# Optimization experiments

Hardware: AMD Instinct MI355X
Metric: run time of the kernel (lower is better)

Reference implementation:

```python
import jax, jax.numpy as jnp
import numpy as np

TOP_K = 2


def setup_inputs() -> dict:
    key = jax.random.key(0)
    k1, k2, k3, k4 = jax.random.split(key, 4)
    B, S, D, F, E = 4, 512, 512, 2048, 16
    hidden_states = jax.random.normal(k1, (B, S, D), dtype=jnp.float32)
    gate_weight = jax.random.normal(k2, (E, D), dtype=jnp.float32) * 0.02
    w1 = jax.random.normal(k3, (E, F, D), dtype=jnp.float32) * 0.02
    w2 = jax.random.normal(k4, (E, D, F), dtype=jnp.float32) * 0.02
    return {"hidden_states": hidden_states, "gate_weight": gate_weight, "w1": w1, "w2": w2}


def reference(hidden_states, gate_weight, w1, w2):
    B, S, D = hidden_states.shape
    E = gate_weight.shape[0]
    x = hidden_states.reshape(-1, D)  # [T, D]

    # fused_top_k_routing: logits = x @ Wg^T, top-k, softmax over the k values
    gate_logits = x @ gate_weight.T  # [T, E]
    top_vals, top_idx = jax.lax.top_k(gate_logits, TOP_K)  # [T, k]
    routing_w = jax.nn.softmax(top_vals, axis=-1)  # [T, k]

    # _prepare_expert_inputs: token t goes to expert e iff e in its top-k
    mask = jnp.any(top_idx[:, :, None] == jnp.arange(E)[None, None, :], axis=1)  # [T, E] bool

    # Expert FFN on routed tokens, computed densely over (token, expert) pairs then masked.
    # h[t,e,f] = silu(x_t @ W1_e^T)
    h = jax.nn.silu(jnp.einsum('td,efd->tef', x, w1))  # [T, E, F]
    counts = jnp.sum(mask, axis=0)  # [E]
    h_sum = jnp.einsum('tef,te->ef', h, mask.astype(h.dtype))  # [E, F]
    h_mean = h_sum / jnp.maximum(counts, 1)[:, None].astype(h.dtype)

    # fused_expert_scatter_gather uses expert_outputs[e].mean(dim=0);
    # mean(W2 @ act) = W2 @ mean(act) since W2 is linear.
    y_mean = jnp.einsum('ef,edf->ed', h_mean, w2)  # [E, D]
    y_mean = jnp.where((counts > 0)[:, None], y_mean, 0.0)

    # per-token combine: sum_k w_k * mean_output[expert_k]
    out = jnp.einsum('tk,tkd->td', routing_w, y_mean[top_idx])  # [T, D]
    return out.reshape(B, S, D)
```

## Files before the change

kernel.cpp:

```cpp
#include <hip/hip_runtime.h>

#define NTOK   2048
#define DIM    512
#define FDIM   2048
#define NEXP   16
#define CAP    768
#define BT2    128
#define NTB    (CAP / BT2)

typedef __bf16 bf16x8 __attribute__((ext_vector_type(8)));
typedef __bf16 bf16x4 __attribute__((ext_vector_type(4)));
typedef float  floatx4 __attribute__((ext_vector_type(4)));

#define WS_COUNTS    0
#define WS_ZEROPAGE  1024
#define WS_TOPIDX    4096
#define WS_ROUTW     20480
#define WS_HMEAN     36864
#define WS_YMEAN     167936
#define WS_XG        200704
#define WS_ZERO_BYTES 167936

__device__ __forceinline__ void async_lds16(const void* g, void* l) {
    __builtin_amdgcn_global_load_lds(
        (__attribute__((address_space(1))) void*)(void*)g,
        (__attribute__((address_space(3))) void*)l, 16, 0, 0);
}

__global__ __launch_bounds__(256) void k1_route_gather(
    const float* __restrict__ x, const float* __restrict__ gw,
    int* __restrict__ counts, int* __restrict__ top_idx,
    float* __restrict__ routw, __bf16* __restrict__ Xg)
{
    __shared__ float xt[16 * DIM];
    __shared__ float lg[16][17];
    __shared__ int   gdst[16][2];
    const int tid = threadIdx.x;
    const int t0  = blockIdx.x * 16;

    {
        const float4* src = (const float4*)(x + (size_t)t0 * DIM);
        float4* dst = (float4*)xt;
        #pragma unroll
        for (int i = 0; i < 8; ++i) dst[i * 256 + tid] = src[i * 256 + tid];
    }
    __syncthreads();

    {
        const int tl = tid >> 4, e = tid & 15;
        const float4* xr = (const float4*)(xt + tl * DIM);
        const float4* gr = (const float4*)(gw + e * DIM);
        float acc = 0.f;
        #pragma unroll 8
        for (int j = 0; j < DIM / 4; ++j) {
            float4 a = xr[j], b = gr[j];
            acc += a.x * b.x + a.y * b.y + a.z * b.z + a.w * b.w;
        }
        lg[tl][e] = acc;
    }
    __syncthreads();

    if (tid < 16) {
        const int tl = tid;
        float v0 = -1e30f, v1 = -1e30f; int i0 = 0, i1 = 0;
        #pragma unroll
        for (int e = 0; e < NEXP; ++e) {
            float v = lg[tl][e];
            if (v > v0)      { v1 = v0; i1 = i0; v0 = v; i0 = e; }
            else if (v > v1) { v1 = v;  i1 = e; }
        }
        float e1 = __expf(v1 - v0);
        float w0 = 1.f / (1.f + e1);
        float w1 = 1.f - w0;
        const int t = t0 + tl;
        top_idx[t * 2]     = i0; top_idx[t * 2 + 1] = i1;
        routw[t * 2]       = w0; routw[t * 2 + 1]   = w1;
        int p0 = atomicAdd(counts + i0, 1);
        int p1 = atomicAdd(counts + i1, 1);
        gdst[tl][0] = (p0 < CAP) ? (i0 * CAP + p0) : -1;
        gdst[tl][1] = (p1 < CAP) ? (i1 * CAP + p1) : -1;
    }
    __syncthreads();

    #pragma unroll
    for (int it = 0; it < 16; ++it) {
        int s   = it * 256 + tid;
        int job = s >> 7, el = s & 127;
        int tl  = job >> 1, k = job & 1;
        int dst = gdst[tl][k];
        if (dst >= 0) {
            float4 v = ((const float4*)(xt + tl * DIM))[el];
            bf16x4 o = { (__bf16)v.x, (__bf16)v.y, (__bf16)v.z, (__bf16)v.w };
            *(bf16x4*)(Xg + (size_t)dst * DIM + el * 4) = o;
        }
    }
}

__global__ __launch_bounds__(256) void k2_expert_ffn(
    const float* __restrict__ w1, const __bf16* __restrict__ Xg,
    const int* __restrict__ counts, const __bf16* __restrict__ zp,
    float* __restrict__ hmean)
{
    __shared__ __align__(16) __bf16 w1s[2][8 * 65 * 8];
    __shared__ __align__(16) __bf16 xs[2][8 * 128 * 8];
    __shared__ float hred[64][2];

    const int tid = threadIdx.x;
    const int bid = blockIdx.x;
    const int tb  = bid >> 9;
    const int rem = bid & 511;
    const int e   = rem & 15;
    const int f0  = (rem >> 4) * 64;
    const int cnt = min(counts[e], CAP);
    if (tb * BT2 >= cnt) return;
    const float inv = 1.f / (float)cnt;

    const int wv   = tid >> 6;
    const int lane = tid & 63;
    const int q    = lane >> 4;
    const int l15  = lane & 15;
    const int fsub = (wv & 1) * 32;
    const int tsub = (wv >> 1) * 64;

    const int wfA = tid >> 3,        wgA = tid & 7;
    const int wfB = (256 + tid) >> 3, wgB = (256 + tid) & 7;
    const float* w1rowA = w1 + ((size_t)(e * FDIM + f0 + wfA)) * DIM + wgA * 8;
    const float* w1rowB = w1 + ((size_t)(e * FDIM + f0 + wfB)) * DIM + wgB * 8;

    float4 wa0, wb0, wa1, wb1;

    auto ISSUE_W1 = [&](int c) {
        const float* pA = w1rowA + c * 64;
        const float* pB = w1rowB + c * 64;
        wa0 = ((const float4*)pA)[0]; wb0 = ((const float4*)pA)[1];
        wa1 = ((const float4*)pB)[0]; wb1 = ((const float4*)pB)[1];
    };
    auto WRITE_W1 = [&](int b) {
        bf16x8 v;
        v[0] = (__bf16)wa0.x; v[1] = (__bf16)wa0.y; v[2] = (__bf16)wa0.z; v[3] = (__bf16)wa0.w;
        v[4] = (__bf16)wb0.x; v[5] = (__bf16)wb0.y; v[6] = (__bf16)wb0.z; v[7] = (__bf16)wb0.w;
        *(bf16x8*)(&w1s[b][0] + ((size_t)wgA * 65 + wfA) * 8) = v;
        v[0] = (__bf16)wa1.x; v[1] = (__bf16)wa1.y; v[2] = (__bf16)wa1.z; v[3] = (__bf16)wa1.w;
        v[4] = (__bf16)wb1.x; v[5] = (__bf16)wb1.y; v[6] = (__bf16)wb1.z; v[7] = (__bf16)wb1.w;
        *(bf16x8*)(&w1s[b][0] + ((size_t)wgB * 65 + wfB) * 8) = v;
    };
    auto STAGE_X = [&](int b, int c) {
        __bf16* dst0 = &xs[b][0];
        #pragma unroll
        for (int it = 0; it < 4; ++it) {
            int base = it * 256 + wv * 64;
            int slot = base + lane;
            int kg = slot >> 7, t = slot & 127;
            int r  = tb * BT2 + t;
            const __bf16* src = (r < cnt)
                ? (Xg + ((size_t)(e * CAP + r)) * DIM + c * 64 + kg * 8)
                : zp;
            async_lds16(src, dst0 + (size_t)base * 8);
        }
    };

    ISSUE_W1(0);
    STAGE_X(0, 0);
    WRITE_W1(0);
    __syncthreads();

    floatx4 acc[2][4];
    #pragma unroll
    for (int a = 0; a < 2; ++a)
        #pragma unroll
        for (int b = 0; b < 4; ++b) acc[a][b] = (floatx4)0.f;

    int cur = 0;
    for (int c = 0; c < 8; ++c) {
        if (c < 7) {
            ISSUE_W1(c + 1);
            STAGE_X(cur ^ 1, c + 1);
        }
        const __bf16* wp = &w1s[cur][0];
        const __bf16* xp = &xs[cur][0];
        #pragma unroll
        for (int ks = 0; ks < 2; ++ks) {
            const int kg = ks * 4 + q;
            bf16x8 a0 = *(const bf16x8*)(wp + ((size_t)kg * 65 + fsub + l15) * 8);
            bf16x8 a1 = *(const bf16x8*)(wp + ((size_t)kg * 65 + fsub + 16 + l15) * 8);
            #pragma unroll
            for (int tt = 0; tt < 4; ++tt) {
                bf16x8 bfr = *(const bf16x8*)(xp + ((size_t)kg * 128 + tsub + tt * 16 + l15) * 8);
                acc[0][tt] = __builtin_amdgcn_mfma_f32_16x16x32_bf16(a0, bfr, acc[0][tt], 0, 0, 0);
                acc[1][tt] = __builtin_amdgcn_mfma_f32_16x16x32_bf16(a1, bfr, acc[1][tt], 0, 0, 0);
            }
        }
        if (c < 7) {
            WRITE_W1(cur ^ 1);
            __syncthreads();
            cur ^= 1;
        }
    }

    float hs[8];
    #pragma unroll
    for (int i = 0; i < 8; ++i) hs[i] = 0.f;
    #pragma unroll
    for (int fa = 0; fa < 2; ++fa)
        #pragma unroll
        for (int tt = 0; tt < 4; ++tt)
            #pragma unroll
            for (int r = 0; r < 4; ++r) {
                float v = acc[fa][tt][r];
                hs[fa * 4 + r] += v / (1.f + __expf(-v));
            }

    #pragma unroll
    for (int i = 0; i < 8; ++i) {
        float v = hs[i];
        v += __shfl_xor(v, 1);
        v += __shfl_xor(v, 2);
        v += __shfl_xor(v, 4);
        v += __shfl_xor(v, 8);
        hs[i] = v;
    }
    if (l15 == 0) {
        #pragma unroll
        for (int fa = 0; fa < 2; ++fa)
            #pragma unroll
            for (int r = 0; r < 4; ++r) {
                int row = fsub + fa * 16 + q * 4 + r;
                hred[row][wv >> 1] = hs[fa * 4 + r];
            }
    }
    __syncthreads();
    if (tid < 64)
        atomicAdd(hmean + (size_t)e * FDIM + f0 + tid,
                  (hred[tid][0] + hred[tid][1]) * inv);
}

__global__ __launch_bounds__(256) void k3_ymean(
    const float* __restrict__ w2, const float* __restrict__ hmean,
    const int* __restrict__ counts, float* __restrict__ ymean)
{
    __shared__ float hl[FDIM];
    const int tid = threadIdx.x;
    const int bid = blockIdx.x;
    const int e   = bid >> 7;
    const int d0  = (bid & 127) * 4;

    {
        const float4* hg = (const float4*)(hmean + (size_t)e * FDIM);
        float4* hl4 = (float4*)hl;
        hl4[tid]       = hg[tid];
        hl4[256 + tid] = hg[256 + tid];
    }
    __syncthreads();

    const int wv = tid >> 6, lane = tid & 63;
    const int d = d0 + wv;
    const float4* wr  = (const float4*)(w2 + ((size_t)e * DIM + d) * FDIM);
    const float4* hl4 = (const float4*)hl;
    float acc = 0.f;
    #pragma unroll
    for (int i = 0; i < 8; ++i) {
        float4 a = wr[i * 64 + lane];
        float4 h = hl4[i * 64 + lane];
        acc += a.x * h.x + a.y * h.y + a.z * h.z + a.w * h.w;
    }
    #pragma unroll
    for (int m = 1; m < 64; m <<= 1) acc += __shfl_xor(acc, m);
    if (lane == 0)
        ymean[e * DIM + d] = (counts[e] > 0) ? acc : 0.f;
}

__global__ __launch_bounds__(256) void k4_combine(
    const int* __restrict__ top_idx, const float* __restrict__ routw,
    const float* __restrict__ ymean, float* __restrict__ out)
{
    const int idx = blockIdx.x * 256 + threadIdx.x;
    const int t = idx >> 7;
    const int c = idx & 127;
    const int i0 = top_idx[t * 2], i1 = top_idx[t * 2 + 1];
    const float w0 = routw[t * 2], w1 = routw[t * 2 + 1];
    float4 a = ((const float4*)(ymean + (size_t)i0 * DIM))[c];
    float4 b = ((const float4*)(ymean + (size_t)i1 * DIM))[c];
    float4 o;
    o.x = w0 * a.x + w1 * b.x;
    o.y = w0 * a.y + w1 * b.y;
    o.z = w0 * a.z + w1 * b.z;
    o.w = w0 * a.w + w1 * b.w;
    ((float4*)out)[idx] = o;
}

extern "C" void kernel_launch(void* const* d_in, const int* in_sizes, int n_in,
                              void* d_out, int out_size, void* d_ws, size_t ws_size,
                              hipStream_t stream)
{
    (void)in_sizes; (void)n_in; (void)out_size; (void)ws_size;
    const float* x  = (const float*)d_in[0];
    const float* gw = (const float*)d_in[1];
    const float* w1 = (const float*)d_in[2];
    const float* w2 = (const float*)d_in[3];
    float* out = (float*)d_out;

    char* ws = (char*)d_ws;
    int*    counts  = (int*)   (ws + WS_COUNTS);
    const __bf16* zp = (const __bf16*)(ws + WS_ZEROPAGE);
    int*    top_idx = (int*)   (ws + WS_TOPIDX);
    float*  routw   = (float*) (ws + WS_ROUTW);
    float*  hmean   = (float*) (ws + WS_HMEAN);
    float*  ymean   = (float*) (ws + WS_YMEAN);
    __bf16* Xg      = (__bf16*)(ws + WS_XG);

    hipMemsetAsync(d_ws, 0, WS_ZERO_BYTES, stream);

    k1_route_gather<<<dim3(NTOK / 16), dim3(256), 0, stream>>>(x, gw, counts, top_idx, routw, Xg);
    k2_expert_ffn  <<<dim3(NTB * 32 * NEXP), dim3(256), 0, stream>>>(w1, Xg, counts, zp, hmean);
    k3_ymean       <<<dim3(NEXP * 128), dim3(256), 0, stream>>>(w2, hmean, counts, ymean);
    k4_combine     <<<dim3(NTOK * DIM / 4 / 256), dim3(256), 0, stream>>>(top_idx, routw, ymean, out);
}
```

Measured before the change: 218.4 us.

## Load W1 fragments directly into registers and remap blocks across XCDs

The W1 tile no longer goes through shared memory. Each lane loads its MFMA A-fragment straight from global fp32, converts it to bf16 in registers and feeds the MFMA directly. This removes the LDS store/load round trip and halves LDS usage. In exchange, W1 rows are duplicated across the two t-sub waves that share an f-sub, and global loads become less coalesced (per-lane strided rows). Block indices are also remapped so that the token-blocks of the same (expert, f) tile land on the same XCD, improving L2 reuse of W1.

New measurement: 258.0 us. +18.2%, slower.

```diff
diff --git a/kernel.cpp b/kernel.cpp
--- a/kernel.cpp
+++ b/kernel.cpp
@@ -101,17 +101,19 @@
     const int* __restrict__ counts, const __bf16* __restrict__ zp,
     float* __restrict__ hmean)
 {
-    __shared__ __align__(16) __bf16 w1s[2][8 * 65 * 8];
     __shared__ __align__(16) __bf16 xs[2][8 * 128 * 8];
     __shared__ float hred[64][2];
 
-    const int tid = threadIdx.x;
-    const int bid = blockIdx.x;
-    const int tb  = bid >> 9;
-    const int rem = bid & 511;
-    const int e   = rem & 15;
-    const int f0  = (rem >> 4) * 64;
-    const int cnt = min(counts[e], CAP);
+    const int tid  = threadIdx.x;
+    const int bid  = blockIdx.x;
+    const int xcd  = bid & 7;
+    const int rest = bid >> 3;
+    const int tb   = rest % NTB;
+    const int tgrp = rest / NTB;
+    const int tile = tgrp * 8 + xcd;
+    const int e    = tile & 15;
+    const int f0   = (tile >> 4) * 64;
+    const int cnt  = min(counts[e], CAP);
     if (tb * BT2 >= cnt) return;
     const float inv = 1.f / (float)cnt;
 
@@ -122,27 +124,29 @@
     const int fsub = (wv & 1) * 32;
     const int tsub = (wv >> 1) * 64;
 
-    const int wfA = tid >> 3,        wgA = tid & 7;
-    const int wfB = (256 + tid) >> 3, wgB = (256 + tid) & 7;
-    const float* w1rowA = w1 + ((size_t)(e * FDIM + f0 + wfA)) * DIM + wgA * 8;
-    const float* w1rowB = w1 + ((size_t)(e * FDIM + f0 + wfB)) * DIM + wgB * 8;
-
-    float4 wa0, wb0, wa1, wb1;
-
-    auto ISSUE_W1 = [&](int c) {
-        const float* pA = w1rowA + c * 64;
-        const float* pB = w1rowB + c * 64;
-        wa0 = ((const float4*)pA)[0]; wb0 = ((const float4*)pA)[1];
-        wa1 = ((const float4*)pB)[0]; wb1 = ((const float4*)pB)[1];
+    const float* arow0 = w1 + ((size_t)(e * FDIM + f0 + fsub + l15)) * DIM + q * 8;
+    const float* arow1 = arow0 + 16 * DIM;
+
+    float4 aw[8];
+    bf16x8 A[2][2];
+
+    auto ISSUE_A = [&](int c) {
+        const float* p0 = arow0 + c * 64;
+        const float* p1 = arow1 + c * 64;
+        aw[0] = ((const float4*)p0)[0];       aw[1] = ((const float4*)p0)[1];
+        aw[2] = ((const float4*)p1)[0];       aw[3] = ((const float4*)p1)[1];
+        aw[4] = ((const float4*)(p0 + 32))[0]; aw[5] = ((const float4*)(p0 + 32))[1];
+        aw[6] = ((const float4*)(p1 + 32))[0]; aw[7] = ((const float4*)(p1 + 32))[1];
     };
-    auto WRITE_W1 = [&](int b) {
-        bf16x8 v;
-        v[0] = (__bf16)wa0.x; v[1] = (__bf16)wa0.y; v[2] = (__bf16)wa0.z; v[3] = (__bf16)wa0.w;
-        v[4] = (__bf16)wb0.x; v[5] = (__bf16)wb0.y; v[6] = (__bf16)wb0.z; v[7] = (__bf16)wb0.w;
-        *(bf16x8*)(&w1s[b][0] + ((size_t)wgA * 65 + wfA) * 8) = v;
-        v[0] = (__bf16)wa1.x; v[1] = (__bf16)wa1.y; v[2] = (__bf16)wa1.z; v[3] = (__bf16)wa1.w;
-        v[4] = (__bf16)wb1.x; v[5] = (__bf16)wb1.y; v[6] = (__bf16)wb1.z; v[7] = (__bf16)wb1.w;
-        *(bf16x8*)(&w1s[b][0] + ((size_t)wgB * 65 + wfB) * 8) = v;
+    auto CVT_A = [&]() {
+        #pragma unroll
+        for (int i = 0; i < 4; ++i) {
+            float4 a = aw[i * 2], b = aw[i * 2 + 1];
+            bf16x8 v;
+            v[0] = (__bf16)a.x; v[1] = (__bf16)a.y; v[2] = (__bf16)a.z; v[3] = (__bf16)a.w;
+            v[4] = (__bf16)b.x; v[5] = (__bf16)b.y; v[6] = (__bf16)b.z; v[7] = (__bf16)b.w;
+            A[i >> 1][i & 1] = v;
+        }
     };
     auto STAGE_X = [&](int b, int c) {
         __bf16* dst0 = &xs[b][0];
@@ -159,9 +163,9 @@
         }
     };
 
-    ISSUE_W1(0);
+    ISSUE_A(0);
     STAGE_X(0, 0);
-    WRITE_W1(0);
+    CVT_A();
     __syncthreads();
 
     floatx4 acc[2][4];
@@ -170,30 +174,26 @@
         #pragma unroll
         for (int b = 0; b < 4; ++b) acc[a][b] = (floatx4)0.f;
 
-    int cur = 0;
+    #pragma unroll
     for (int c = 0; c < 8; ++c) {
         if (c < 7) {
-            ISSUE_W1(c + 1);
-            STAGE_X(cur ^ 1, c + 1);
-        }
-        const __bf16* wp = &w1s[cur][0];
-        const __bf16* xp = &xs[cur][0];
+            ISSUE_A(c + 1);
+            STAGE_X((c + 1) & 1, c + 1);
+        }
+        const __bf16* xp = &xs[c & 1][0];
         #pragma unroll
         for (int ks = 0; ks < 2; ++ks) {
             const int kg = ks * 4 + q;
-            bf16x8 a0 = *(const bf16x8*)(wp + ((size_t)kg * 65 + fsub + l15) * 8);
-            bf16x8 a1 = *(const bf16x8*)(wp + ((size_t)kg * 65 + fsub + 16 + l15) * 8);
             #pragma unroll
             for (int tt = 0; tt < 4; ++tt) {
                 bf16x8 bfr = *(const bf16x8*)(xp + ((size_t)kg * 128 + tsub + tt * 16 + l15) * 8);
-                acc[0][tt] = __builtin_amdgcn_mfma_f32_16x16x32_bf16(a0, bfr, acc[0][tt], 0, 0, 0);
-                acc[1][tt] = __builtin_amdgcn_mfma_f32_16x16x32_bf16(a1, bfr, acc[1][tt], 0, 0, 0);
+                acc[0][tt] = __builtin_amdgcn_mfma_f32_16x16x32_bf16(A[ks][0], bfr, acc[0][tt], 0, 0, 0);
+                acc[1][tt] = __builtin_amdgcn_mfma_f32_16x16x32_bf16(A[ks][1], bfr, acc[1][tt], 0, 0, 0);
             }
         }
         if (c < 7) {
-            WRITE_W1(cur ^ 1);
+            CVT_A();
             __syncthreads();
-            cur ^= 1;
         }
     }
 
```
